# Kernel optimization log

Hardware: AMD Instinct MI355X
Metric: run time of the kernel (lower is better)

Reference implementation:

```python
import jax, jax.numpy as jnp
import numpy as np

NEG_INF = -9e15


def setup_inputs() -> dict:
    key = jax.random.key(0)
    k1, k2, k3, k4, k5 = jax.random.split(key, 5)
    N, F_IN, F_OUT = 8192, 512, 256
    x = jax.random.normal(k1, (N, F_IN), dtype=jnp.float32)
    adjacent_matrix = jax.random.randint(k2, (N, N), 0, 2, dtype=jnp.int32)
    # xavier-normal-like scales (gain sqrt(2))
    W = jax.random.normal(k3, (F_IN, F_OUT), dtype=jnp.float32) * np.sqrt(2.0) * np.sqrt(2.0 / (F_IN + F_OUT))
    a1 = jax.random.normal(k4, (F_OUT, 1), dtype=jnp.float32) * np.sqrt(2.0) * np.sqrt(2.0 / (F_OUT + 1))
    a2 = jax.random.normal(k5, (F_OUT, 1), dtype=jnp.float32) * np.sqrt(2.0) * np.sqrt(2.0 / (F_OUT + 1))
    return {"x": x, "adjacent_matrix": adjacent_matrix, "W": W, "a1": a1, "a2": a2}


def reference(x, adjacent_matrix, W, a1, a2):
    alpha = 0.2  # LeakyReLU negative slope
    h = x @ W                                   # [N, F_out]
    f1 = h @ a1                                 # [N, 1]
    f2 = h @ a2                                 # [N, 1]
    e = f1 + f2.T                               # [N, N] broadcast pairwise scores
    e = jnp.where(e > 0, e, alpha * e)          # LeakyReLU
    e = jnp.where(adjacent_matrix > 0, e, NEG_INF)  # mask non-edges
    attention = jax.nn.softmax(e, axis=1)       # [N, N]
    h_prime = attention @ h                     # [N, F_out]
    return jax.nn.elu(h_prime)                  # concat=True -> ELU
```

## Files before the change

kernel.cpp:

```cpp
#include <hip/hip_runtime.h>
#include <hip/hip_bf16.h>

#define N_NODES 8192
#define F_IN 512
#define F_OUT 256
#define KSPLIT 4
#define KCHUNK (N_NODES / KSPLIT)

using short8 = __attribute__((ext_vector_type(8))) short;
using f32x4  = __attribute__((ext_vector_type(4))) float;

typedef __attribute__((address_space(3))) void lds_t;
typedef const __attribute__((address_space(1))) void gbl_t;

__device__ __forceinline__ short f2bf(float v) {
    union { float f; unsigned u; } x; x.f = v;
    unsigned r = x.u + 0x7fffu + ((x.u >> 16) & 1u);
    return (short)(r >> 16);
}

__global__ void k_prep(const float* __restrict__ W, const float* __restrict__ a1,
                       const float* __restrict__ a2, float* __restrict__ w1,
                       float* __restrict__ w2, short* __restrict__ WTg) {
    const int k = blockIdx.x;
    const int l = threadIdx.x;
    float4 wv = *(const float4*)(W + (size_t)k * F_OUT + 4 * l);
    float4 av = *(const float4*)(a1 + 4 * l);
    float4 bv = *(const float4*)(a2 + 4 * l);
    float s1 = wv.x*av.x + wv.y*av.y + wv.z*av.z + wv.w*av.w;
    float s2 = wv.x*bv.x + wv.y*bv.y + wv.z*bv.z + wv.w*bv.w;
    WTg[(size_t)(4*l+0)*F_IN + k] = f2bf(wv.x);
    WTg[(size_t)(4*l+1)*F_IN + k] = f2bf(wv.y);
    WTg[(size_t)(4*l+2)*F_IN + k] = f2bf(wv.z);
    WTg[(size_t)(4*l+3)*F_IN + k] = f2bf(wv.w);
    #pragma unroll
    for (int off = 32; off; off >>= 1) {
        s1 += __shfl_down(s1, off);
        s2 += __shfl_down(s2, off);
    }
    if (l == 0) { w1[k] = s1; w2[k] = s2; }
}

__global__ void k_f12(const float* __restrict__ x, const float* __restrict__ w1,
                      const float* __restrict__ w2, float* __restrict__ f1,
                      float* __restrict__ f2) {
    const int wv = threadIdx.x >> 6, l = threadIdx.x & 63;
    const int i = blockIdx.x * 4 + wv;
    const float* xr = x + (size_t)i * F_IN;
    float s1 = 0.f, s2 = 0.f;
    #pragma unroll
    for (int t = 0; t < 2; ++t) {
        int k = t * 256 + l * 4;
        float4 xv = *(const float4*)(xr + k);
        float4 u  = *(const float4*)(w1 + k);
        float4 v  = *(const float4*)(w2 + k);
        s1 += xv.x*u.x + xv.y*u.y + xv.z*u.z + xv.w*u.w;
        s2 += xv.x*v.x + xv.y*v.y + xv.z*v.z + xv.w*v.w;
    }
    #pragma unroll
    for (int off = 32; off; off >>= 1) {
        s1 += __shfl_down(s1, off);
        s2 += __shfl_down(s2, off);
    }
    if (l == 0) { f1[i] = s1; f2[i] = s2; }
}

__launch_bounds__(256)
__global__ void k_hT(const float* __restrict__ x, const short* __restrict__ WTg,
                     short* __restrict__ hTs) {
    __shared__ short x_lds[32 * 64];
    __shared__ short wt_lds[256 * 64];
    const int tid = threadIdx.x;
    const int wv = tid >> 6, l = tid & 63, lg = l >> 4, lr = l & 15;
    const int ibase = blockIdx.x * 32;
    f32x4 acc[4][2];
    #pragma unroll
    for (int a = 0; a < 4; ++a)
        #pragma unroll
        for (int b = 0; b < 2; ++b) acc[a][b] = (f32x4){0.f, 0.f, 0.f, 0.f};
    for (int k0 = 0; k0 < F_IN; k0 += 64) {
        __syncthreads();
        {
            int i = tid >> 3, ch = tid & 7;
            const float* src = x + (size_t)(ibase + i) * F_IN + k0 + ch * 8;
            float4 v0 = *(const float4*)(src);
            float4 v1 = *(const float4*)(src + 4);
            short8 s;
            s[0]=f2bf(v0.x); s[1]=f2bf(v0.y); s[2]=f2bf(v0.z); s[3]=f2bf(v0.w);
            s[4]=f2bf(v1.x); s[5]=f2bf(v1.y); s[6]=f2bf(v1.z); s[7]=f2bf(v1.w);
            *(short8*)&x_lds[i * 64 + 8 * (ch ^ (i & 7))] = s;
        }
        {
            int cb = tid >> 3, ch = tid & 7;
            #pragma unroll
            for (int p = 0; p < 8; ++p) {
                int c = cb + 32 * p;
                short8 s = *(const short8*)(WTg + (size_t)c * F_IN + k0 + ch * 8);
                *(short8*)&wt_lds[c * 64 + 8 * (ch ^ (c & 7))] = s;
            }
        }
        __syncthreads();
        #pragma unroll
        for (int ks = 0; ks < 2; ++ks) {
            short8 bfrag[2], afrag[4];
            #pragma unroll
            for (int it = 0; it < 2; ++it) {
                int i = it * 16 + lr;
                bfrag[it] = *(short8*)&x_lds[i * 64 + 8 * ((lg + 4*ks) ^ (i & 7))];
            }
            #pragma unroll
            for (int ct = 0; ct < 4; ++ct) {
                int c = wv * 64 + ct * 16 + lr;
                afrag[ct] = *(short8*)&wt_lds[c * 64 + 8 * ((lg + 4*ks) ^ (c & 7))];
            }
            #pragma unroll
            for (int ct = 0; ct < 4; ++ct)
                #pragma unroll
                for (int it = 0; it < 2; ++it)
                    acc[ct][it] = __builtin_amdgcn_mfma_f32_16x16x32_bf16(
                        afrag[ct], bfrag[it], acc[ct][it], 0, 0, 0);
        }
    }
    #pragma unroll
    for (int ct = 0; ct < 4; ++ct)
        #pragma unroll
        for (int it = 0; it < 2; ++it)
            #pragma unroll
            for (int r = 0; r < 4; ++r) {
                int c = wv * 64 + ct * 16 + 4 * lg + r;
                int i = ibase + it * 16 + lr;
                int isw = (i & ~56) | ((((i >> 3) & 7) ^ (c & 7)) << 3);
                hTs[(size_t)c * N_NODES + isw] = f2bf(acc[ct][it][r]);
            }
}

__launch_bounds__(256, 2)
__global__ void k_attn(const int* __restrict__ adj, const short* __restrict__ hTs,
                       const float* __restrict__ f1, const float* __restrict__ f2,
                       float* __restrict__ part, float* __restrict__ psum) {
    __shared__ short h_lds[2 * 16384];
    const int tid = threadIdx.x;
    const int wv = tid >> 6, l = tid & 63, lg = l >> 4, lr = l & 15;
    const int ksid = blockIdx.x & 3;
    const int rowblk = blockIdx.x >> 2;
    const int r0 = rowblk * 64;
    const int myrow = r0 + wv * 16 + lr;
    const short* hsrc = hTs + (size_t)(tid >> 3) * N_NODES + (tid & 7) * 8;
    const int q = l & 3, srow = wv * 16 + (l >> 2);
    const int* asrc = adj + (size_t)(r0 + srow) * N_NODES + q * 16;
    const float f1v = f1[myrow];
    const float L2E = 1.44269504f;
    f32x4 acc[16];
    #pragma unroll
    for (int t = 0; t < 16; ++t) acc[t] = (f32x4){0.f, 0.f, 0.f, 0.f};
    float ps = 0.f;
    const int kbeg = ksid * KCHUNK;
    const int kend = kbeg + KCHUNK;

    int4 AA[4], BA[4];

#define STAGE(BUFOFF, K0) do {                                                  \
    _Pragma("unroll")                                                           \
    for (int p = 0; p < 8; ++p)                                                 \
        __builtin_amdgcn_global_load_lds(                                       \
            (gbl_t*)(hsrc + (size_t)p * 32 * N_NODES + (K0)),                   \
            (lds_t*)&h_lds[(BUFOFF) + p * 2048 + wv * 512], 16, 0, 0);          \
} while (0)

#define ADJLOAD(A, K0) do {                                                     \
    _Pragma("unroll")                                                           \
    for (int p = 0; p < 4; ++p) A[p] = *(const int4*)(asrc + (K0) + p * 4);     \
} while (0)

#define COMPUTE_KS(K0, BUFOFF, AMV, KS) do {                                    \
    const int kg = (K0) + 32 * (KS) + 8 * lg;                                   \
    const unsigned mbyte = ((AMV) >> (8 * (lg & 1))) & 0xffu;                   \
    const float4 fa = *(const float4*)(f2 + kg);                                \
    const float4 fb4 = *(const float4*)(f2 + kg + 4);                           \
    const float f2v[8] = {fa.x, fa.y, fa.z, fa.w, fb4.x, fb4.y, fb4.z, fb4.w};  \
    short8 pa;                                                                  \
    _Pragma("unroll")                                                           \
    for (int j = 0; j < 8; ++j) {                                               \
        float ee = f1v + f2v[j];                                                \
        float le = fmaxf(ee, 0.2f * ee);                                        \
        float pv = (mbyte & (1u << j)) ? exp2f(fminf(le * L2E, 80.f)) : 0.f;    \
        ps += pv;                                                               \
        pa[j] = f2bf(pv);                                                       \
    }                                                                           \
    const int swz = 8 * ((lg + 4 * (KS)) ^ (lr & 7));                           \
    __builtin_amdgcn_s_setprio(1);                                              \
    _Pragma("unroll")                                                           \
    for (int t = 0; t < 16; ++t) {                                              \
        short8 bfrag = *(short8*)&h_lds[(BUFOFF) + t * 1024 + lr * 64 + swz];   \
        acc[t] = __builtin_amdgcn_mfma_f32_16x16x32_bf16(pa, bfrag, acc[t], 0, 0, 0); \
    }                                                                           \
    __builtin_amdgcn_s_setprio(0);                                              \
} while (0)

#define COMPUTE(K0, BUFOFF, A) do {                                             \
    unsigned m = 0;                                                             \
    _Pragma("unroll")                                                           \
    for (int p = 0; p < 4; ++p) {                                               \
        m |= (A[p].x > 0 ? 1u : 0u) << (4 * p);                                 \
        m |= (A[p].y > 0 ? 2u : 0u) << (4 * p);                                 \
        m |= (A[p].z > 0 ? 4u : 0u) << (4 * p);                                 \
        m |= (A[p].w > 0 ? 8u : 0u) << (4 * p);                                 \
    }                                                                           \
    const unsigned am0 = (unsigned)__shfl((int)m, (lr << 2) | (lg >> 1));       \
    const unsigned am1 = (unsigned)__shfl((int)m, (lr << 2) | 2 | (lg >> 1));   \
    COMPUTE_KS(K0, BUFOFF, am0, 0);                                             \
    COMPUTE_KS(K0, BUFOFF, am1, 1);                                             \
} while (0)

    STAGE(0, kbeg);
    ADJLOAD(AA, kbeg);
    __syncthreads();
    for (int k0 = kbeg; k0 < kend; k0 += 128) {
        STAGE(16384, k0 + 64);
        ADJLOAD(BA, k0 + 64);
        COMPUTE(k0, 0, AA);
        __syncthreads();
        if (k0 + 128 < kend) {
            STAGE(0, k0 + 128);
            ADJLOAD(AA, k0 + 128);
        }
        COMPUTE(k0 + 64, 16384, BA);
        __syncthreads();
    }
#undef STAGE
#undef ADJLOAD
#undef COMPUTE
#undef COMPUTE_KS

    ps += __shfl_xor(ps, 16);
    ps += __shfl_xor(ps, 32);
    if (lg == 0) psum[ksid * N_NODES + myrow] = ps;
    float* pb = part + (size_t)ksid * N_NODES * F_OUT;
    #pragma unroll
    for (int t = 0; t < 16; ++t)
        #pragma unroll
        for (int r = 0; r < 4; ++r) {
            int row = r0 + wv * 16 + 4 * lg + r;
            int c = t * 16 + lr;
            pb[(size_t)row * F_OUT + c] = acc[t][r];
        }
}

__global__ void k_comb(const float* __restrict__ part, const float* __restrict__ psum,
                       float* __restrict__ out) {
    const int i = blockIdx.x, c = threadIdx.x;
    float o = 0.f, s = 0.f;
    #pragma unroll
    for (int qq = 0; qq < KSPLIT; ++qq) {
        o += part[(size_t)qq * N_NODES * F_OUT + (size_t)i * F_OUT + c];
        s += psum[qq * N_NODES + i];
    }
    float v = o / s;
    out[(size_t)i * F_OUT + c] = (v > 0.f) ? v : expm1f(v);
}

extern "C" void kernel_launch(void* const* d_in, const int* in_sizes, int n_in,
                              void* d_out, int out_size, void* d_ws, size_t ws_size,
                              hipStream_t stream) {
    const float* x  = (const float*)d_in[0];
    const int* adj  = (const int*)d_in[1];
    const float* W  = (const float*)d_in[2];
    const float* a1 = (const float*)d_in[3];
    const float* a2 = (const float*)d_in[4];
    float* out = (float*)d_out;

    short* hTs = (short*)d_ws;
    short* WTg = hTs + (size_t)F_OUT * N_NODES;
    float* fb  = (float*)(WTg + (size_t)F_OUT * F_IN);
    float* w1   = fb;
    float* w2   = fb + 512;
    float* f1   = fb + 1024;
    float* f2   = fb + 1024 + N_NODES;
    float* part = fb + 32768;
    float* psum = part + (size_t)KSPLIT * N_NODES * F_OUT;

    k_prep<<<F_IN, 64, 0, stream>>>(W, a1, a2, w1, w2, WTg);
    k_f12<<<N_NODES / 4, 256, 0, stream>>>(x, w1, w2, f1, f2);
    k_hT<<<N_NODES / 32, 256, 0, stream>>>(x, WTg, hTs);
    k_attn<<<128 * KSPLIT, 256, 0, stream>>>(adj, hTs, f1, f2, part, psum);
    k_comb<<<N_NODES, 256, 0, stream>>>(part, psum, out);
}
```

Baseline: 448.9 us.

## Deepen attention pipeline to 4-stage ring with 32-wide tiles and counted waits

Restructures the attention main loop from a 2-buffer, 64-column double-buffer into a 4-slot LDS ring of 32-column tiles. H tiles are staged two ahead and adjacency loads four ahead, and a vmcnt-based wait plus a single raw barrier per tile replaces the two full syncthreads per iteration. f2 is preloaded into LDS once per block, and the swizzle moves from the h producer kernel into the load addressing. The goal is to hide global latency better and cut barrier stalls, at the cost of more registers for in-flight adjacency data and a fragile hand-tuned wait count.

```diff
diff --git a/kernel.cpp b/kernel.cpp
--- a/kernel.cpp
+++ b/kernel.cpp
@@ -6,6 +6,7 @@
 #define F_OUT 256
 #define KSPLIT 4
 #define KCHUNK (N_NODES / KSPLIT)
+#define NTILES (KCHUNK / 32)
 
 using short8 = __attribute__((ext_vector_type(8))) short;
 using f32x4  = __attribute__((ext_vector_type(4))) float;
@@ -67,7 +68,7 @@
 
 __launch_bounds__(256)
 __global__ void k_hT(const float* __restrict__ x, const short* __restrict__ WTg,
-                     short* __restrict__ hTs) {
+                     short* __restrict__ hT) {
     __shared__ short x_lds[32 * 64];
     __shared__ short wt_lds[256 * 64];
     const int tid = threadIdx.x;
@@ -129,108 +130,113 @@
             for (int r = 0; r < 4; ++r) {
                 int c = wv * 64 + ct * 16 + 4 * lg + r;
                 int i = ibase + it * 16 + lr;
-                int isw = (i & ~56) | ((((i >> 3) & 7) ^ (c & 7)) << 3);
-                hTs[(size_t)c * N_NODES + isw] = f2bf(acc[ct][it][r]);
+                hT[(size_t)c * N_NODES + i] = f2bf(acc[ct][it][r]);
             }
 }
 
 __launch_bounds__(256, 2)
-__global__ void k_attn(const int* __restrict__ adj, const short* __restrict__ hTs,
+__global__ void k_attn(const int* __restrict__ adj, const short* __restrict__ hT,
                        const float* __restrict__ f1, const float* __restrict__ f2,
                        float* __restrict__ part, float* __restrict__ psum) {
-    __shared__ short h_lds[2 * 16384];
+    __shared__ short h_lds[4 * 8192];
+    __shared__ float f2_lds[KCHUNK];
     const int tid = threadIdx.x;
     const int wv = tid >> 6, l = tid & 63, lg = l >> 4, lr = l & 15;
     const int ksid = blockIdx.x & 3;
     const int rowblk = blockIdx.x >> 2;
     const int r0 = rowblk * 64;
     const int myrow = r0 + wv * 16 + lr;
-    const short* hsrc = hTs + (size_t)(tid >> 3) * N_NODES + (tid & 7) * 8;
+    const int kbeg = ksid * KCHUNK;
+    const short* hsrcb = hT + (size_t)(wv * 16 + (l >> 2)) * N_NODES
+                            + ((l & 3) ^ ((l >> 3) & 3)) * 8 + kbeg;
     const int q = l & 3, srow = wv * 16 + (l >> 2);
-    const int* asrc = adj + (size_t)(r0 + srow) * N_NODES + q * 16;
+    const int* asrcb = adj + (size_t)(r0 + srow) * N_NODES + q * 8 + kbeg;
     const float f1v = f1[myrow];
     const float L2E = 1.44269504f;
+    const int rdoff = lr * 32 + (lg ^ ((lr >> 1) & 3)) * 8;
     f32x4 acc[16];
     #pragma unroll
     for (int t = 0; t < 16; ++t) acc[t] = (f32x4){0.f, 0.f, 0.f, 0.f};
     float ps = 0.f;
-    const int kbeg = ksid * KCHUNK;
-    const int kend = kbeg + KCHUNK;
-
-    int4 AA[4], BA[4];
-
-#define STAGE(BUFOFF, K0) do {                                                  \
+
+    int4 S0[2], S1[2], S2[2], S3[2];
+    unsigned mA, mB;
+
+#define STAGE(T) do {                                                           \
     _Pragma("unroll")                                                           \
-    for (int p = 0; p < 8; ++p)                                                 \
+    for (int p = 0; p < 4; ++p)                                                 \
         __builtin_amdgcn_global_load_lds(                                       \
-            (gbl_t*)(hsrc + (size_t)p * 32 * N_NODES + (K0)),                   \
-            (lds_t*)&h_lds[(BUFOFF) + p * 2048 + wv * 512], 16, 0, 0);          \
-} while (0)
-
-#define ADJLOAD(A, K0) do {                                                     \
-    _Pragma("unroll")                                                           \
-    for (int p = 0; p < 4; ++p) A[p] = *(const int4*)(asrc + (K0) + p * 4);     \
-} while (0)
-
-#define COMPUTE_KS(K0, BUFOFF, AMV, KS) do {                                    \
-    const int kg = (K0) + 32 * (KS) + 8 * lg;                                   \
-    const unsigned mbyte = ((AMV) >> (8 * (lg & 1))) & 0xffu;                   \
-    const float4 fa = *(const float4*)(f2 + kg);                                \
-    const float4 fb4 = *(const float4*)(f2 + kg + 4);                           \
+            (gbl_t*)(hsrcb + (size_t)p * 64 * N_NODES + (T) * 32),              \
+            (lds_t*)&h_lds[((T) & 3) * 8192 + p * 2048 + wv * 512], 16, 0, 0);  \
+} while (0)
+
+#define ADJ(S, T) do {                                                          \
+    S[0] = *(const int4*)(asrcb + (T) * 32);                                    \
+    S[1] = *(const int4*)(asrcb + (T) * 32 + 4);                                \
+} while (0)
+
+#define PACK(MD, S) do {                                                        \
+    unsigned _m = (S[0].x > 0 ? 1u : 0u) | (S[0].y > 0 ? 2u : 0u) |             \
+                  (S[0].z > 0 ? 4u : 0u) | (S[0].w > 0 ? 8u : 0u) |             \
+                  (S[1].x > 0 ? 16u : 0u) | (S[1].y > 0 ? 32u : 0u) |           \
+                  (S[1].z > 0 ? 64u : 0u) | (S[1].w > 0 ? 128u : 0u);           \
+    MD = (unsigned)__shfl((int)_m, (lr << 2) | lg);                             \
+} while (0)
+
+#define COMPUTE(T, MB) do {                                                     \
+    const int bo = ((T) & 3) * 8192;                                            \
+    const float4 fa = *(const float4*)&f2_lds[(T) * 32 + lg * 8];               \
+    const float4 fb4 = *(const float4*)&f2_lds[(T) * 32 + lg * 8 + 4];          \
     const float f2v[8] = {fa.x, fa.y, fa.z, fa.w, fb4.x, fb4.y, fb4.z, fb4.w};  \
     short8 pa;                                                                  \
     _Pragma("unroll")                                                           \
     for (int j = 0; j < 8; ++j) {                                               \
         float ee = f1v + f2v[j];                                                \
         float le = fmaxf(ee, 0.2f * ee);                                        \
-        float pv = (mbyte & (1u << j)) ? exp2f(fminf(le * L2E, 80.f)) : 0.f;    \
+        float pv = ((MB) & (1u << j)) ? exp2f(fminf(le * L2E, 80.f)) : 0.f;     \
         ps += pv;                                                               \
         pa[j] = f2bf(pv);                                                       \
     }                                                                           \
-    const int swz = 8 * ((lg + 4 * (KS)) ^ (lr & 7));                           \
     __builtin_amdgcn_s_setprio(1);                                              \
     _Pragma("unroll")                                                           \
-    for (int t = 0; t < 16; ++t) {                                              \
-        short8 bfrag = *(short8*)&h_lds[(BUFOFF) + t * 1024 + lr * 64 + swz];   \
-        acc[t] = __builtin_amdgcn_mfma_f32_16x16x32_bf16(pa, bfrag, acc[t], 0, 0, 0); \
+    for (int t16 = 0; t16 < 16; ++t16) {                                        \
+        short8 bfrag = *(short8*)&h_lds[bo + t16 * 512 + rdoff];                \
+        acc[t16] = __builtin_amdgcn_mfma_f32_16x16x32_bf16(pa, bfrag, acc[t16], 0, 0, 0); \
     }                                                                           \
     __builtin_amdgcn_s_setprio(0);                                              \
 } while (0)
 
-#define COMPUTE(K0, BUFOFF, A) do {                                             \
-    unsigned m = 0;                                                             \
-    _Pragma("unroll")                                                           \
-    for (int p = 0; p < 4; ++p) {                                               \
-        m |= (A[p].x > 0 ? 1u : 0u) << (4 * p);                                 \
-        m |= (A[p].y > 0 ? 2u : 0u) << (4 * p);                                 \
-        m |= (A[p].z > 0 ? 4u : 0u) << (4 * p);                                 \
-        m |= (A[p].w > 0 ? 8u : 0u) << (4 * p);                                 \
-    }                                                                           \
-    const unsigned am0 = (unsigned)__shfl((int)m, (lr << 2) | (lg >> 1));       \
-    const unsigned am1 = (unsigned)__shfl((int)m, (lr << 2) | 2 | (lg >> 1));   \
-    COMPUTE_KS(K0, BUFOFF, am0, 0);                                             \
-    COMPUTE_KS(K0, BUFOFF, am1, 1);                                             \
-} while (0)
-
-    STAGE(0, kbeg);
-    ADJLOAD(AA, kbeg);
+#define BODY(T, SL, SP, MU, MP) do {                                            \
+    PACK(MP, SP);                                        \
+    if ((T) + 4 < NTILES) ADJ(SL, (T) + 4);                                     \
+    if ((T) + 2 < NTILES) STAGE((T) + 2);                                       \
+    asm volatile("s_waitcnt vmcnt(12)" ::: "memory");                           \
+    __builtin_amdgcn_s_barrier();                                               \
+    __builtin_amdgcn_sched_barrier(0);                                          \
+    COMPUTE(T, MU);                                                             \
+} while (0)
+
+    {
+        int i8 = tid * 8;
+        *(float4*)&f2_lds[i8]     = *(const float4*)(f2 + kbeg + i8);
+        *(float4*)&f2_lds[i8 + 4] = *(const float4*)(f2 + kbeg + i8 + 4);
+    }
+    ADJ(S0, 0); ADJ(S1, 1); ADJ(S2, 2); ADJ(S3, 3);
+    STAGE(0); STAGE(1);
+    PACK(mA, S0);
     __syncthreads();
-    for (int k0 = kbeg; k0 < kend; k0 += 128) {
-        STAGE(16384, k0 + 64);
-        ADJLOAD(BA, k0 + 64);
-        COMPUTE(k0, 0, AA);
-        __syncthreads();
-        if (k0 + 128 < kend) {
-            STAGE(0, k0 + 128);
-            ADJLOAD(AA, k0 + 128);
-        }
-        COMPUTE(k0 + 64, 16384, BA);
-        __syncthreads();
+
+    for (int t = 0; t < NTILES; t += 4) {
+        BODY(t + 0, S0, S1, mA, mB);
+        BODY(t + 1, S1, S2, mB, mA);
+        BODY(t + 2, S2, S3, mA, mB);
+        BODY(t + 3, S3, S0, mB, mA);
     }
 #undef STAGE
-#undef ADJLOAD
+#undef ADJ
+#undef PACK
 #undef COMPUTE
-#undef COMPUTE_KS
+#undef BODY
 
     ps += __shfl_xor(ps, 16);
     ps += __shfl_xor(ps, 32);
@@ -269,8 +275,8 @@
     const float* a2 = (const float*)d_in[4];
     float* out = (float*)d_out;
 
-    short* hTs = (short*)d_ws;
-    short* WTg = hTs + (size_t)F_OUT * N_NODES;
+    short* hT  = (short*)d_ws;
+    short* WTg = hT + (size_t)F_OUT * N_NODES;
     float* fb  = (float*)(WTg + (size_t)F_OUT * F_IN);
     float* w1   = fb;
     float* w2   = fb + 512;
@@ -281,7 +287,7 @@
 
     k_prep<<<F_IN, 64, 0, stream>>>(W, a1, a2, w1, w2, WTg);
     k_f12<<<N_NODES / 4, 256, 0, stream>>>(x, w1, w2, f1, f2);
-    k_hT<<<N_NODES / 32, 256, 0, stream>>>(x, WTg, hTs);
-    k_attn<<<128 * KSPLIT, 256, 0, stream>>>(adj, hTs, f1, f2, part, psum);
+    k_hT<<<N_NODES / 32, 256, 0, stream>>>(x, WTg, hT);
+    k_attn<<<128 * KSPLIT, 256, 0, stream>>>(adj, hT, f1, f2, part, psum);
     k_comb<<<N_NODES, 256, 0, stream>>>(part, psum, out);
 }
```

Measured after the change: 437.9 us. -2.4%, faster.
